# Kernel optimization log

Measured on AMD Instinct MI355X. Metric: run time of the kernel, lower is better.

Reference implementation:

```python
import jax, jax.numpy as jnp
import numpy as np

EMBED_DIM = 1024
N_HEADS = 16


def setup_inputs() -> dict:
    key = jax.random.key(0)
    k1, k2, k3 = jax.random.split(key, 3)
    B, T, C = 4, 2048, EMBED_DIM
    x0 = jax.random.normal(k1, (B, T, C), dtype=jnp.float32)
    # Linear weights stored as (in, out) so y = x @ W, matching torch Linear math.
    w_attn = jax.random.normal(k2, (C, 3 * C), dtype=jnp.float32) * (1.0 / np.sqrt(C))
    w_proj = jax.random.normal(k3, (C, C), dtype=jnp.float32) * (1.0 / np.sqrt(C))
    return {"x0": x0, "w_attn": w_attn, "w_proj": w_proj}


def reference(x0, w_attn, w_proj):
    B, T, C = x0.shape
    H = N_HEADS
    D = C // H  # head dim
    qkv = x0 @ w_attn                      # [B, T, 3C]
    q, k, v = jnp.split(qkv, 3, axis=-1)
    # [B, T, C] -> [B, H, T, D]
    q = q.reshape(B, T, H, D).transpose(0, 2, 1, 3)
    k = k.reshape(B, T, H, D).transpose(0, 2, 1, 3)
    v = v.reshape(B, T, H, D).transpose(0, 2, 1, 3)
    scale = 1.0 / np.sqrt(D)
    attn = jnp.einsum('bhqd,bhkd->bhqk', q, k) * scale  # [B, H, T, T]
    causal = jnp.tril(jnp.ones((T, T), dtype=bool))
    attn = jnp.where(causal[None, None, :, :], attn, -jnp.inf)
    attn = jax.nn.softmax(attn, axis=-1)
    y = jnp.einsum('bhqk,bhkd->bhqd', attn, v)           # [B, H, T, D]
    y = y.transpose(0, 2, 1, 3).reshape(B, T, C)
    return y @ w_proj
```

## Files before the change

### kernel.cpp

```cpp
#include <hip/hip_runtime.h>

#define TSEQ 2048
#define NB 4
#define NH 16
#define HD 64
#define CEMB 1024
#define MROWS (NB*TSEQ)

typedef _Float16 half8 __attribute__((ext_vector_type(8)));
typedef _Float16 half4_t __attribute__((ext_vector_type(4)));
typedef float floatx4 __attribute__((ext_vector_type(4)));

__device__ __forceinline__ floatx4 mfma16x32(half8 a, half8 b, floatx4 c) {
    return __builtin_amdgcn_mfma_f32_16x16x32_f16(a, b, c, 0, 0, 0);
}

__device__ __forceinline__ void async16(const _Float16* g, _Float16* l) {
    __builtin_amdgcn_global_load_lds((const __attribute__((address_space(1))) void*)g,
                                     (__attribute__((address_space(3))) void*)l, 16, 0, 0);
}

__global__ __launch_bounds__(256) void cvt_fp32_fp16(const float* __restrict__ in,
                                                     _Float16* __restrict__ out) {
    size_t i = ((size_t)blockIdx.x * 256 + threadIdx.x) * 8;
    float4 a = *(const float4*)(in + i);
    float4 b = *(const float4*)(in + i + 4);
    half8 h;
    h[0] = (_Float16)a.x; h[1] = (_Float16)a.y; h[2] = (_Float16)a.z; h[3] = (_Float16)a.w;
    h[4] = (_Float16)b.x; h[5] = (_Float16)b.y; h[6] = (_Float16)b.z; h[7] = (_Float16)b.w;
    *(half8*)(out + i) = h;
}

__global__ __launch_bounds__(256) void transpose_cvt(const float* __restrict__ in,
                                                     _Float16* __restrict__ out,
                                                     int R, int Ccols) {
    __shared__ float tile[32][33];
    int bx = blockIdx.x;
    int by = blockIdx.y;
    int tx = threadIdx.x, ty = threadIdx.y;
    int x = bx * 32 + tx;
#pragma unroll
    for (int i = 0; i < 32; i += 8) {
        int y = by * 32 + ty + i;
        tile[ty + i][tx] = in[(size_t)y * Ccols + x];
    }
    __syncthreads();
#pragma unroll
    for (int i = 0; i < 32; i += 8) {
        int oc = bx * 32 + ty + i;
        int orow = by * 32 + tx;
        out[(size_t)oc * R + orow] = (_Float16)tile[tx][ty + i];
    }
}

template<int MODE>
__global__ __launch_bounds__(512, 4) void gemm_nt(const _Float16* __restrict__ A,
                                                  const _Float16* __restrict__ Bt,
                                                  float* __restrict__ Cf,
                                                  _Float16* __restrict__ Ch,
                                                  _Float16* __restrict__ VTh,
                                                  int N, int K) {
    __shared__ __align__(16) _Float16 As[2][8192];
    __shared__ __align__(16) _Float16 Bs[2][4096];

    const int tid = threadIdx.x;
    const int wv = tid >> 6, lane = tid & 63;
    const int wm = wv & 3, wn = wv >> 2;
    const int l16 = lane & 15, lq = lane >> 4;

    const int pid = blockIdx.x + gridDim.x * blockIdx.y;
    const int nn = gridDim.y;
    const int pig = 8 * nn;
    const int gid = pid / pig;
    const int rem = pid - gid * pig;
    const int bm = gid * 8 + (rem & 7);
    const int bn = rem >> 3;

    const int srow = lane >> 2;
    const int scol = ((lane & 3) ^ ((lane >> 3) & 3)) * 8;
    const _Float16* Abase = A + (size_t)(bm * 256) * K;
    const _Float16* Bbase = Bt + (size_t)(bn * 128) * K;

    const floatx4 zero = {0.f, 0.f, 0.f, 0.f};
    floatx4 acc[4][4];
#pragma unroll
    for (int i = 0; i < 4; i++)
#pragma unroll
        for (int j = 0; j < 4; j++) acc[i][j] = zero;

    auto stage = [&](int bf, int k0) {
#pragma unroll
        for (int cc = 0; cc < 2; cc++) {
            const int c = wv * 2 + cc;
            const size_t gofs = (size_t)(c * 16 + srow) * K + k0 + scol;
            async16(Abase + gofs, &As[bf][c * 512]);
        }
        {
            const int c = wv;
            const size_t gofs = (size_t)(c * 16 + srow) * K + k0 + scol;
            async16(Bbase + gofs, &Bs[bf][c * 512]);
        }
    };

    stage(0, 0);
    int buf = 0;
    const int sw = (lq ^ ((l16 >> 1) & 3)) * 8;
    for (int k0 = 0; k0 < K; k0 += 32) {
        __syncthreads();
        if (k0 + 32 < K) stage(buf ^ 1, k0 + 32);
        half8 af[4], bf[4];
#pragma unroll
        for (int i = 0; i < 4; i++) {
            af[i] = *(const half8*)&As[buf][(wm * 64 + i * 16 + l16) * 32 + sw];
            bf[i] = *(const half8*)&Bs[buf][(wn * 64 + i * 16 + l16) * 32 + sw];
        }
#pragma unroll
        for (int i = 0; i < 4; i++)
#pragma unroll
            for (int j = 0; j < 4; j++)
                acc[i][j] = mfma16x32(af[i], bf[j], acc[i][j]);
        buf ^= 1;
    }

    if (MODE == 1) {
#pragma unroll
        for (int i = 0; i < 4; i++) {
            int row = bm * 256 + wm * 64 + i * 16 + lq * 4;
#pragma unroll
            for (int j = 0; j < 4; j++) {
                int col = bn * 128 + wn * 64 + j * 16 + l16;
#pragma unroll
                for (int r = 0; r < 4; r++)
                    Cf[(size_t)(row + r) * N + col] = acc[i][j][r];
            }
        }
    } else {
        const int which = bn >> 3;
        if (which < 2) {
#pragma unroll
            for (int j = 0; j < 4; j++) {
                int n = bn * 128 + wn * 64 + j * 16 + l16;
                int c = n & 1023, h = c >> 6, d = c & 63;
                _Float16* dst = Ch + (size_t)which * ((size_t)MROWS * CEMB)
                                   + (size_t)h * (TSEQ * HD) + d;
#pragma unroll
                for (int i = 0; i < 4; i++) {
                    int row = bm * 256 + wm * 64 + i * 16 + lq * 4;
#pragma unroll
                    for (int r = 0; r < 4; r++) {
                        int m = row + r;
                        int b = m >> 11, t = m & 2047;
                        dst[(size_t)b * (NH * TSEQ * HD) + (size_t)t * HD] = (_Float16)acc[i][j][r];
                    }
                }
            }
        } else {
#pragma unroll
            for (int j = 0; j < 4; j++) {
                int n = bn * 128 + wn * 64 + j * 16 + l16;
                int c = n & 1023, h = c >> 6, d = c & 63;
#pragma unroll
                for (int i = 0; i < 4; i++) {
                    int m0 = bm * 256 + wm * 64 + i * 16 + lq * 4;
                    int b = m0 >> 11, t = m0 & 2047;
                    half4_t pk;
#pragma unroll
                    for (int r = 0; r < 4; r++) pk[r] = (_Float16)acc[i][j][r];
                    *(half4_t*)&VTh[(((size_t)(b * NH + h)) * HD + d) * TSEQ + t] = pk;
                }
            }
        }
    }
}

__global__ __launch_bounds__(256, 4) void attn_fwd(const _Float16* __restrict__ Qg,
                                                   const _Float16* __restrict__ Kg,
                                                   const _Float16* __restrict__ VTg,
                                                   _Float16* __restrict__ Y) {
    __shared__ __align__(16) _Float16 Ks[2][4096];
    __shared__ __align__(16) _Float16 Vt[2][4096];

    const int tid = threadIdx.x;
    const int w = tid >> 6, lane = tid & 63;
    const int l16 = lane & 15, quad = lane >> 4;
    const int bh = blockIdx.y;
    const int xq = blockIdx.x;
    const int b = bh >> 4, h = bh & 15;
    const int qt = (b == 0) ? xq
                 : (b == 1) ? (15 - xq)
                 : (b == 2) ? ((xq + 8) & 15)
                            : ((7 - xq) & 15);

    const _Float16* Qb = Qg + (size_t)bh * TSEQ * HD;
    const _Float16* Kb = Kg + (size_t)bh * TSEQ * HD;
    const _Float16* Vb = VTg + (size_t)bh * HD * TSEQ;

    const _Float16 ksc = (_Float16)(0.125f * 1.44269504089f);
    const floatx4 zero = {0.f, 0.f, 0.f, 0.f};

    half8 qf[2][2];
#pragma unroll
    for (int g = 0; g < 2; g++) {
        const _Float16* qrow = Qb + (size_t)(qt * 128 + g * 64 + w * 16 + l16) * HD;
        qf[g][0] = *(const half8*)(qrow + quad * 8);
        qf[g][1] = *(const half8*)(qrow + 32 + quad * 8);
#pragma unroll
        for (int e = 0; e < 8; e++) { qf[g][0][e] *= ksc; qf[g][1][e] *= ksc; }
    }

    floatx4 o[2][4];
#pragma unroll
    for (int g = 0; g < 2; g++)
#pragma unroll
        for (int dt = 0; dt < 4; dt++) o[g][dt] = zero;
    float lsum[2] = {0.f, 0.f};

    const int srow8 = lane >> 3;
    const int scol8 = ((lane & 7) ^ (lane >> 3)) * 8;

    auto stage = [&](int bf, int kt2) {
#pragma unroll
        for (int cc = 0; cc < 2; cc++) {
            const int c = w * 2 + cc;
            const int row = c * 8 + srow8;
            async16(Kb + (size_t)(kt2 * 64 + row) * HD + scol8, &Ks[bf][c * 512]);
            async16(Vb + (size_t)row * TSEQ + kt2 * 64 + scol8, &Vt[bf][c * 512]);
        }
    };

    const int kmax = 2 * qt + 1;
    stage(0, 0);
    int buf = 0;
    for (int kt = 0; kt <= kmax; ++kt) {
        __syncthreads();
        if (kt < kmax) stage(buf ^ 1, kt + 1);

        half8 kf0[4], kf1[4];
#pragma unroll
        for (int nj = 0; nj < 4; nj++) {
            const int rb = (nj * 16 + l16) * 64;
            kf0[nj] = *(const half8*)&Ks[buf][rb + ((quad ^ (l16 & 7)) * 8)];
            kf1[nj] = *(const half8*)&Ks[buf][rb + (((quad ^ 4) ^ (l16 & 7)) * 8)];
        }

        const bool doA = (kt <= 2 * qt);
        half8 pf[2][2];
#pragma unroll
        for (int g = 0; g < 2; g++) {
            if (g == 0 && !doA) continue;
            floatx4 st[4];
#pragma unroll
            for (int nj = 0; nj < 4; nj++) {
                floatx4 t = mfma16x32(kf0[nj], qf[g][0], zero);
                st[nj] = mfma16x32(kf1[nj], qf[g][1], t);
            }
            if (kt * 64 + 63 > qt * 128 + g * 64 + w * 16) {
                const int klim = qt * 128 + g * 64 + w * 16 + l16 - kt * 64;
#pragma unroll
                for (int nj = 0; nj < 4; nj++)
#pragma unroll
                    for (int r = 0; r < 4; r++) {
                        int key = nj * 16 + quad * 4 + r;
                        if (key > klim) st[nj][r] = -1e30f;
                    }
            }
#pragma unroll
            for (int nj = 0; nj < 4; nj++)
#pragma unroll
                for (int r = 0; r < 4; r++) {
                    float p = __builtin_amdgcn_exp2f(st[nj][r]);
                    lsum[g] += p;
                    pf[g][nj >> 1][(nj & 1) * 4 + r] = (_Float16)p;
                }
        }

#pragma unroll
        for (int u = 0; u < 2; u++) {
#pragma unroll
            for (int dt = 0; dt < 4; dt++) {
                const int rb = (dt * 16 + l16) * 64;
                const int g0 = u * 4 + (quad >> 1);
                const int sub = (quad & 1) * 4;
                half4_t lo = *(const half4_t*)&Vt[buf][rb + ((g0 ^ (l16 & 7)) * 8 + sub)];
                half4_t hi = *(const half4_t*)&Vt[buf][rb + (((g0 + 2) ^ (l16 & 7)) * 8 + sub)];
                half8 vf;
                vf[0] = lo[0]; vf[1] = lo[1]; vf[2] = lo[2]; vf[3] = lo[3];
                vf[4] = hi[0]; vf[5] = hi[1]; vf[6] = hi[2]; vf[7] = hi[3];
                if (doA) o[0][dt] = mfma16x32(pf[0][u], vf, o[0][dt]);
                o[1][dt] = mfma16x32(pf[1][u], vf, o[1][dt]);
            }
        }
        buf ^= 1;
    }

#pragma unroll
    for (int g = 0; g < 2; g++) {
        float lt = lsum[g];
        lt += __shfl_xor(lt, 16);
        lt += __shfl_xor(lt, 32);
        float linv[4];
#pragma unroll
        for (int r = 0; r < 4; r++) linv[r] = 1.0f / __shfl(lt, quad * 4 + r);
#pragma unroll
        for (int dt = 0; dt < 4; dt++)
#pragma unroll
            for (int r = 0; r < 4; r++) {
                int q = qt * 128 + g * 64 + w * 16 + quad * 4 + r;
                int d = dt * 16 + l16;
                Y[((size_t)(b * TSEQ + q)) * CEMB + h * HD + d] = (_Float16)(o[g][dt][r] * linv[r]);
            }
    }
}

extern "C" void kernel_launch(void* const* d_in, const int* in_sizes, int n_in,
                              void* d_out, int out_size, void* d_ws, size_t ws_size,
                              hipStream_t stream) {
    const float* x0     = (const float*)d_in[0];
    const float* w_attn = (const float*)d_in[1];
    const float* w_proj = (const float*)d_in[2];
    float* out = (float*)d_out;

    _Float16* xh  = (_Float16*)d_ws;
    _Float16* wqt = xh  + (size_t)MROWS * CEMB;
    _Float16* wpt = wqt + (size_t)3 * CEMB * CEMB;
    _Float16* qh  = wpt + (size_t)CEMB * CEMB;
    _Float16* kh  = qh  + (size_t)MROWS * CEMB;
    _Float16* vt  = kh  + (size_t)MROWS * CEMB;
    _Float16* yh  = vt  + (size_t)MROWS * CEMB;

    cvt_fp32_fp16<<<(MROWS * CEMB) / (256 * 8), 256, 0, stream>>>(x0, xh);
    transpose_cvt<<<dim3(3 * CEMB / 32, CEMB / 32), dim3(32, 8), 0, stream>>>(w_attn, wqt, CEMB, 3 * CEMB);
    transpose_cvt<<<dim3(CEMB / 32, CEMB / 32), dim3(32, 8), 0, stream>>>(w_proj, wpt, CEMB, CEMB);

    gemm_nt<0><<<dim3(MROWS / 256, 3 * CEMB / 128), 512, 0, stream>>>(xh, wqt, nullptr, qh, vt, 3 * CEMB, CEMB);
    attn_fwd<<<dim3(TSEQ / 128, NB * NH), 256, 0, stream>>>(qh, kh, vt, yh);
    gemm_nt<1><<<dim3(MROWS / 256, CEMB / 128), 512, 0, stream>>>(yh, wpt, out, nullptr, nullptr, CEMB, CEMB);
}
```

Baseline: 256.6 us.

## Double attention query tile to 256 rows and use 128-row tiles for output projection

The attention kernel now handles 256 query rows per block with 8 waves instead of 128 rows with 4 waves. Each staged K/V tile is therefore shared by twice as many queries, and the causal load-balancing permutation over query tiles is simplified. The output projection GEMM is templated to a 128x128 tile with 256 threads, which doubles its grid count to fill more CUs. The trade-offs are fewer attention blocks (512), a coarser causal imbalance, and more B reloads in the smaller GEMM.

```diff
diff --git a/kernel.cpp b/kernel.cpp
--- a/kernel.cpp
+++ b/kernel.cpp
@@ -53,19 +53,20 @@
     }
 }
 
-template<int MODE>
-__global__ __launch_bounds__(512, 4) void gemm_nt(const _Float16* __restrict__ A,
-                                                  const _Float16* __restrict__ Bt,
-                                                  float* __restrict__ Cf,
-                                                  _Float16* __restrict__ Ch,
-                                                  _Float16* __restrict__ VTh,
-                                                  int N, int K) {
-    __shared__ __align__(16) _Float16 As[2][8192];
+template<int MODE, int BM>
+__global__ __launch_bounds__(BM * 2, 4) void gemm_nt(const _Float16* __restrict__ A,
+                                                     const _Float16* __restrict__ Bt,
+                                                     float* __restrict__ Cf,
+                                                     _Float16* __restrict__ Ch,
+                                                     _Float16* __restrict__ VTh,
+                                                     int N, int K) {
+    __shared__ __align__(16) _Float16 As[2][BM * 32];
     __shared__ __align__(16) _Float16 Bs[2][4096];
 
     const int tid = threadIdx.x;
     const int wv = tid >> 6, lane = tid & 63;
-    const int wm = wv & 3, wn = wv >> 2;
+    const int wm = (BM == 256) ? (wv & 3) : (wv >> 1);
+    const int wn = (BM == 256) ? (wv >> 2) : (wv & 1);
     const int l16 = lane & 15, lq = lane >> 4;
 
     const int pid = blockIdx.x + gridDim.x * blockIdx.y;
@@ -78,7 +79,7 @@
 
     const int srow = lane >> 2;
     const int scol = ((lane & 3) ^ ((lane >> 3) & 3)) * 8;
-    const _Float16* Abase = A + (size_t)(bm * 256) * K;
+    const _Float16* Abase = A + (size_t)(bm * BM) * K;
     const _Float16* Bbase = Bt + (size_t)(bn * 128) * K;
 
     const floatx4 zero = {0.f, 0.f, 0.f, 0.f};
@@ -95,10 +96,17 @@
             const size_t gofs = (size_t)(c * 16 + srow) * K + k0 + scol;
             async16(Abase + gofs, &As[bf][c * 512]);
         }
-        {
+        if (BM == 256) {
             const int c = wv;
             const size_t gofs = (size_t)(c * 16 + srow) * K + k0 + scol;
             async16(Bbase + gofs, &Bs[bf][c * 512]);
+        } else {
+#pragma unroll
+            for (int cc = 0; cc < 2; cc++) {
+                const int c = wv * 2 + cc;
+                const size_t gofs = (size_t)(c * 16 + srow) * K + k0 + scol;
+                async16(Bbase + gofs, &Bs[bf][c * 512]);
+            }
         }
     };
 
@@ -125,7 +133,7 @@
     if (MODE == 1) {
 #pragma unroll
         for (int i = 0; i < 4; i++) {
-            int row = bm * 256 + wm * 64 + i * 16 + lq * 4;
+            int row = bm * BM + wm * 64 + i * 16 + lq * 4;
 #pragma unroll
             for (int j = 0; j < 4; j++) {
                 int col = bn * 128 + wn * 64 + j * 16 + l16;
@@ -145,7 +153,7 @@
                                    + (size_t)h * (TSEQ * HD) + d;
 #pragma unroll
                 for (int i = 0; i < 4; i++) {
-                    int row = bm * 256 + wm * 64 + i * 16 + lq * 4;
+                    int row = bm * BM + wm * 64 + i * 16 + lq * 4;
 #pragma unroll
                     for (int r = 0; r < 4; r++) {
                         int m = row + r;
@@ -161,7 +169,7 @@
                 int c = n & 1023, h = c >> 6, d = c & 63;
 #pragma unroll
                 for (int i = 0; i < 4; i++) {
-                    int m0 = bm * 256 + wm * 64 + i * 16 + lq * 4;
+                    int m0 = bm * BM + wm * 64 + i * 16 + lq * 4;
                     int b = m0 >> 11, t = m0 & 2047;
                     half4_t pk;
 #pragma unroll
@@ -173,7 +181,7 @@
     }
 }
 
-__global__ __launch_bounds__(256, 4) void attn_fwd(const _Float16* __restrict__ Qg,
+__global__ __launch_bounds__(512, 4) void attn_fwd(const _Float16* __restrict__ Qg,
                                                    const _Float16* __restrict__ Kg,
                                                    const _Float16* __restrict__ VTg,
                                                    _Float16* __restrict__ Y) {
@@ -184,12 +192,9 @@
     const int w = tid >> 6, lane = tid & 63;
     const int l16 = lane & 15, quad = lane >> 4;
     const int bh = blockIdx.y;
-    const int xq = blockIdx.x;
+    const int x = blockIdx.x;
     const int b = bh >> 4, h = bh & 15;
-    const int qt = (b == 0) ? xq
-                 : (b == 1) ? (15 - xq)
-                 : (b == 2) ? ((xq + 8) & 15)
-                            : ((7 - xq) & 15);
+    const int qt = (b < 2) ? x : (7 - x);
 
     const _Float16* Qb = Qg + (size_t)bh * TSEQ * HD;
     const _Float16* Kb = Kg + (size_t)bh * TSEQ * HD;
@@ -201,7 +206,7 @@
     half8 qf[2][2];
 #pragma unroll
     for (int g = 0; g < 2; g++) {
-        const _Float16* qrow = Qb + (size_t)(qt * 128 + g * 64 + w * 16 + l16) * HD;
+        const _Float16* qrow = Qb + (size_t)(qt * 256 + g * 128 + w * 16 + l16) * HD;
         qf[g][0] = *(const half8*)(qrow + quad * 8);
         qf[g][1] = *(const half8*)(qrow + 32 + quad * 8);
 #pragma unroll
@@ -219,16 +224,12 @@
     const int scol8 = ((lane & 7) ^ (lane >> 3)) * 8;
 
     auto stage = [&](int bf, int kt2) {
-#pragma unroll
-        for (int cc = 0; cc < 2; cc++) {
-            const int c = w * 2 + cc;
-            const int row = c * 8 + srow8;
-            async16(Kb + (size_t)(kt2 * 64 + row) * HD + scol8, &Ks[bf][c * 512]);
-            async16(Vb + (size_t)row * TSEQ + kt2 * 64 + scol8, &Vt[bf][c * 512]);
-        }
+        const int row = w * 8 + srow8;
+        async16(Kb + (size_t)(kt2 * 64 + row) * HD + scol8, &Ks[bf][w * 512]);
+        async16(Vb + (size_t)row * TSEQ + kt2 * 64 + scol8, &Vt[bf][w * 512]);
     };
 
-    const int kmax = 2 * qt + 1;
+    const int kmax = 4 * qt + 3;
     stage(0, 0);
     int buf = 0;
     for (int kt = 0; kt <= kmax; ++kt) {
@@ -243,7 +244,7 @@
             kf1[nj] = *(const half8*)&Ks[buf][rb + (((quad ^ 4) ^ (l16 & 7)) * 8)];
         }
 
-        const bool doA = (kt <= 2 * qt);
+        const bool doA = (kt <= 4 * qt + 1);
         half8 pf[2][2];
 #pragma unroll
         for (int g = 0; g < 2; g++) {
@@ -254,8 +255,8 @@
                 floatx4 t = mfma16x32(kf0[nj], qf[g][0], zero);
                 st[nj] = mfma16x32(kf1[nj], qf[g][1], t);
             }
-            if (kt * 64 + 63 > qt * 128 + g * 64 + w * 16) {
-                const int klim = qt * 128 + g * 64 + w * 16 + l16 - kt * 64;
+            if (kt * 64 + 63 > qt * 256 + g * 128 + w * 16) {
+                const int klim = qt * 256 + g * 128 + w * 16 + l16 - kt * 64;
 #pragma unroll
                 for (int nj = 0; nj < 4; nj++)
 #pragma unroll
@@ -305,7 +306,7 @@
         for (int dt = 0; dt < 4; dt++)
 #pragma unroll
             for (int r = 0; r < 4; r++) {
-                int q = qt * 128 + g * 64 + w * 16 + quad * 4 + r;
+                int q = qt * 256 + g * 128 + w * 16 + quad * 4 + r;
                 int d = dt * 16 + l16;
                 Y[((size_t)(b * TSEQ + q)) * CEMB + h * HD + d] = (_Float16)(o[g][dt][r] * linv[r]);
             }
@@ -332,7 +333,7 @@
     transpose_cvt<<<dim3(3 * CEMB / 32, CEMB / 32), dim3(32, 8), 0, stream>>>(w_attn, wqt, CEMB, 3 * CEMB);
     transpose_cvt<<<dim3(CEMB / 32, CEMB / 32), dim3(32, 8), 0, stream>>>(w_proj, wpt, CEMB, CEMB);
 
-    gemm_nt<0><<<dim3(MROWS / 256, 3 * CEMB / 128), 512, 0, stream>>>(xh, wqt, nullptr, qh, vt, 3 * CEMB, CEMB);
-    attn_fwd<<<dim3(TSEQ / 128, NB * NH), 256, 0, stream>>>(qh, kh, vt, yh);
-    gemm_nt<1><<<dim3(MROWS / 256, CEMB / 128), 512, 0, stream>>>(yh, wpt, out, nullptr, nullptr, CEMB, CEMB);
-}
+    gemm_nt<0, 256><<<dim3(MROWS / 256, 3 * CEMB / 128), 512, 0, stream>>>(xh, wqt, nullptr, qh, vt, 3 * CEMB, CEMB);
+    attn_fwd<<<dim3(TSEQ / 256, NB * NH), 512, 0, stream>>>(qh, kh, vt, yh);
+    gemm_nt<1, 128><<<dim3(MROWS / 128, CEMB / 128), 256, 0, stream>>>(yh, wpt, out, nullptr, nullptr, CEMB, CEMB);
+}
```

Result: faster. 249.1 us (-3.0%).
